# Optimization experiments

Hardware: AMD Instinct MI355X
Metric: run time of the kernel (lower is better)

Reference implementation:

```python
import jax, jax.numpy as jnp
import numpy as np

K_NEIGHBORS = 16
BN_EPS = 1e-5


def _bn(h, g, b):
    # train-mode BatchNorm1d over (batch, points) per channel, biased variance
    mu = h.mean(axis=(0, 1))
    var = h.var(axis=(0, 1))
    return g * (h - mu) * jax.lax.rsqrt(var + BN_EPS) + b


def _gather(arr, idx):
    # arr: [B,N,D], idx: [B,N,K] -> [B,N,K,D]
    return jax.vmap(lambda a, i: a[i])(arr, idx)


def setup_inputs() -> dict:
    key = jax.random.key(0)
    ks = jax.random.split(key, 16)
    B, N, Cin, C, H, M = 4, 4096, 64, 64, 32, 4
    rn = lambda k, s: jax.random.normal(k, s, dtype=jnp.float32) * 0.05
    return {
        "x": jax.random.normal(ks[0], (B, N, Cin), dtype=jnp.float32),
        "p": jax.random.normal(ks[1], (B, N, 3), dtype=jnp.float32),
        "fc1_w": rn(ks[2], (Cin, C)), "fc1_b": jnp.zeros((C,), jnp.float32),
        "bn1_g": jnp.ones((C,), jnp.float32), "bn1_b": jnp.zeros((C,), jnp.float32),
        "qkv_w": rn(ks[3], (C, 3 * C)),
        "pos_w1": rn(ks[4], (3, H)), "pos_b1": jnp.zeros((H,), jnp.float32),
        "pos_w2": rn(ks[5], (H, C)), "pos_b2": jnp.zeros((C,), jnp.float32),
        "attn_w1": rn(ks[6], (C, M * C)), "attn_b1": jnp.zeros((M * C,), jnp.float32),
        "attn_w2": rn(ks[7], (M * C, C)), "attn_b2": jnp.zeros((C,), jnp.float32),
        "bn2_g": jnp.ones((C,), jnp.float32), "bn2_b": jnp.zeros((C,), jnp.float32),
        "fc2_w": rn(ks[8], (C, C)), "fc2_b": jnp.zeros((C,), jnp.float32),
        "bn3_g": jnp.ones((C,), jnp.float32), "bn3_b": jnp.zeros((C,), jnp.float32),
    }


def reference(x, p, fc1_w, fc1_b, bn1_g, bn1_b, qkv_w,
              pos_w1, pos_b1, pos_w2, pos_b2,
              attn_w1, attn_b1, attn_w2, attn_b2,
              bn2_g, bn2_b, fc2_w, fc2_b, bn3_g, bn3_b):
    C = fc1_w.shape[1]
    # fc1 -> BN -> ReLU
    h = jax.nn.relu(_bn(x @ fc1_w + fc1_b, bn1_g, bn1_b))
    residual = h

    # PointTransformerLayer (vector attention over kNN; mask is all-ones)
    qkv = h @ qkv_w  # [B,N,3C]
    q, k, v = qkv[..., :C], qkv[..., C:2 * C], qkv[..., 2 * C:]
    # squared pairwise distances (matches norm-based topk ranking)
    sq = jnp.sum(p * p, axis=-1)  # [B,N]
    d2 = sq[:, :, None] + sq[:, None, :] - 2.0 * jnp.einsum('bnd,bmd->bnm', p, p)
    _, idx = jax.lax.top_k(-d2, K_NEIGHBORS)  # k smallest distances, [B,N,K]

    kj = _gather(k, idx)          # [B,N,K,C]
    vj = _gather(v, idx)          # [B,N,K,C]
    pj = _gather(p, idx)          # [B,N,K,3]

    rel_pos = p[:, :, None, :] - pj                      # [B,N,K,3]
    pe = jax.nn.relu(rel_pos @ pos_w1 + pos_b1) @ pos_w2 + pos_b2  # [B,N,K,C]

    qk_rel = q[:, :, None, :] - kj                       # [B,N,K,C]
    vv = vj + pe
    sim = jax.nn.relu((qk_rel + pe) @ attn_w1 + attn_b1) @ attn_w2 + attn_b2
    attn = jax.nn.softmax(sim, axis=2)                   # softmax over neighbors
    agg = jnp.sum(attn * vv, axis=2)                     # [B,N,C]

    h2 = jax.nn.relu(_bn(agg, bn2_g, bn2_b))
    y = jax.nn.relu(_bn((h2 + residual) @ fc2_w + fc2_b, bn3_g, bn3_b))
    return (y, p)
```

## Files before the change

### kernel.cpp

```cpp
#include <hip/hip_runtime.h>
#include <math.h>

constexpr int kB = 4, kN = 4096, kK = 16;
constexpr int kRows = kB * kN;
constexpr float kEps = 1e-5f;
constexpr float kFltMax = 3.402823466e38f;
constexpr int kCap = 240;

typedef __attribute__((ext_vector_type(8))) short short8;
typedef __attribute__((ext_vector_type(4))) float f32x4;

__device__ __forceinline__ unsigned short f2bf(float x) {
  return (unsigned short)((__float_as_uint(x) + 0x8000u) >> 16);
}
__device__ __forceinline__ unsigned int pkbf(float lo, float hi) {
  return ((__float_as_uint(lo) + 0x8000u) >> 16) |
         ((__float_as_uint(hi) + 0x8000u) & 0xffff0000u);
}
__device__ __forceinline__ float bflo(unsigned int u) { return __uint_as_float(u << 16); }
__device__ __forceinline__ float bfhi(unsigned int u) { return __uint_as_float(u & 0xffff0000u); }
__device__ __forceinline__ float bfu16(unsigned short us) {
  return __uint_as_float(((unsigned int)us) << 16);
}
__device__ __forceinline__ short8 pack8f(float4 a, float4 b) {
  union { unsigned int u[4]; short8 s; } pk;
  pk.u[0] = pkbf(a.x, a.y);
  pk.u[1] = pkbf(a.z, a.w);
  pk.u[2] = pkbf(b.x, b.y);
  pk.u[3] = pkbf(b.z, b.w);
  return pk.s;
}

__device__ __forceinline__ int lane_prefix(unsigned long long m) {
  return __builtin_amdgcn_mbcnt_hi((unsigned)(m >> 32),
         __builtin_amdgcn_mbcnt_lo((unsigned)m, 0));
}

__device__ __forceinline__ void bitonic64(float& sv, int& si, int lane) {
  #pragma unroll
  for (int k = 2; k <= 64; k <<= 1) {
    #pragma unroll
    for (int j = k >> 1; j > 0; j >>= 1) {
      float ov = __shfl_xor(sv, j);
      int   oi = __shfl_xor(si, j);
      bool up = ((lane & k) == 0);
      bool lower = ((lane & j) == 0);
      bool osm = (ov < sv) || (ov == sv && oi < si);
      bool take = (lower == up) ? osm : !osm;
      if (take) { sv = ov; si = oi; }
    }
  }
}

__device__ __forceinline__ float d2q(const float4& Q, const float4& C) {
  float dt = fmaf(Q.z, C.z, fmaf(Q.y, C.y, Q.x * C.x));
  return fmaf(-2.0f, dt, Q.w + C.w);
}

__global__ __launch_bounds__(256) void fc1_conv_kernel(
    const float* __restrict__ x, const float* __restrict__ w,
    const float* __restrict__ bias,
    const float* __restrict__ aw1, const float* __restrict__ aw2,
    const float* __restrict__ pw2, const float* __restrict__ qw,
    const float* __restrict__ f2w,
    const float* __restrict__ pin, float* __restrict__ p4o,
    unsigned short* __restrict__ wpak,
    float* __restrict__ out) {
  __shared__ unsigned short wf[8 * 512];
  const int t = threadIdx.x;
  const int blk = blockIdx.x;
  {
    int id = blk * 256 + t;
    if (id < 16384) {
      int j = id & 7, lane = (id >> 3) & 63, rest = id >> 9;
      int mt = rest >> 1, hh = rest & 1;
      wpak[id] = f2bf(aw1[(32 * hh + 8 * (lane >> 4) + j) * 256 + mt * 16 + (lane & 15)]);
      float3 pp = *reinterpret_cast<const float3*>(pin + 3 * id);
      float4 o;
      o.x = pp.x; o.y = pp.y; o.z = pp.z;
      o.w = pp.x * pp.x + pp.y * pp.y + pp.z * pp.z;
      *reinterpret_cast<float4*>(p4o + 4 * id) = o;
    } else if (id < 32768) {
      int i = id - 16384;
      int j = i & 7, lane = (i >> 3) & 63, rest = i >> 9;
      int ct = rest >> 3, f = rest & 7;
      wpak[id] = f2bf(aw2[(32 * f + 8 * (lane >> 4) + j) * 64 + ct * 16 + (lane & 15)]);
    } else if (id < 34816) {
      int i = id - 32768;
      int c = i >> 5, hh = i & 31;
      wpak[id] = f2bf(pw2[hh * 64 + c]);
    } else if (id < 47104) {
      int i = id - 34816;
      int j = i & 7, lane = (i >> 3) & 63, rest = i >> 9;
      int ct = rest >> 1, hh = rest & 1;
      wpak[id] = f2bf(qw[(32 * hh + 8 * (lane >> 4) + j) * 192 + ct * 16 + (lane & 15)]);
    } else if (id < 51200) {
      int i = id - 47104;
      int j = i & 7, lane = (i >> 3) & 63, rest = i >> 9;
      int ct = rest >> 1, hh = rest & 1;
      wpak[id] = f2bf(f2w[(32 * hh + 8 * (lane >> 4) + j) * 64 + ct * 16 + (lane & 15)]);
    }
  }
  for (int i = t; i < 4096; i += 256) {
    int j = i & 7, lane = (i >> 3) & 63, rest = i >> 9;
    int ct = rest >> 1, hh = rest & 1;
    wf[i] = f2bf(w[(32 * hh + 8 * (lane >> 4) + j) * 64 + ct * 16 + (lane & 15)]);
  }
  __syncthreads();
  const int lane = t & 63, wv = t >> 6;
  const int l = lane & 15, q = lane >> 4;
  const int r0 = blk * 64;
  const int row = r0 + wv * 16 + l;
  const f32x4 zero = {0.f, 0.f, 0.f, 0.f};
  float4 xa0 = *reinterpret_cast<const float4*>(&x[row * 64 + q * 8]);
  float4 xa1 = *reinterpret_cast<const float4*>(&x[row * 64 + q * 8 + 4]);
  float4 xb0 = *reinterpret_cast<const float4*>(&x[row * 64 + 32 + q * 8]);
  float4 xb1 = *reinterpret_cast<const float4*>(&x[row * 64 + 32 + q * 8 + 4]);
  short8 a0 = pack8f(xa0, xa1), a1 = pack8f(xb0, xb1);
  #pragma unroll
  for (int ct = 0; ct < 4; ++ct) {
    short8 b0 = *reinterpret_cast<const short8*>(&wf[(ct * 2 + 0) * 512 + lane * 8]);
    short8 b1 = *reinterpret_cast<const short8*>(&wf[(ct * 2 + 1) * 512 + lane * 8]);
    f32x4 acc = __builtin_amdgcn_mfma_f32_16x16x32_bf16(a0, b0, zero, 0, 0, 0);
    acc = __builtin_amdgcn_mfma_f32_16x16x32_bf16(a1, b1, acc, 0, 0, 0);
    const float bc = bias[ct * 16 + l];
    #pragma unroll
    for (int i = 0; i < 4; ++i)
      out[(r0 + wv * 16 + q * 4 + i) * 64 + ct * 16 + l] = acc[i] + bc;
  }
}

__global__ void stats_part_kernel(const float* __restrict__ src, float* __restrict__ part) {
  __shared__ float sb[256], sb2[256];
  const int t = threadIdx.x, blk = blockIdx.x;
  const int c = t & 63, rg = t >> 6;
  float s = 0.f, s2 = 0.f;
  for (int r = rg; r < 64; r += 4) {
    float v = src[(blk * 64 + r) * 64 + c];
    s += v; s2 += v * v;
  }
  sb[t] = s; sb2[t] = s2; __syncthreads();
  if (t < 64) {
    float ts  = sb[t] + sb[64 + t] + sb[128 + t] + sb[192 + t];
    float ts2 = sb2[t] + sb2[64 + t] + sb2[128 + t] + sb2[192 + t];
    part[blk * 128 + t] = ts;
    part[blk * 128 + 64 + t] = ts2;
  }
}

__global__ void stats_fin_kernel(const float* __restrict__ part,
                                 const float* __restrict__ g, const float* __restrict__ b,
                                 float* __restrict__ A, float* __restrict__ Bv) {
  const int c = threadIdx.x;
  double s = 0.0, s2 = 0.0;
  for (int i = 0; i < 256; ++i) { s += part[i * 128 + c]; s2 += part[i * 128 + 64 + c]; }
  double mean = s / (double)kRows;
  double var = s2 / (double)kRows - mean * mean;
  float rs = (float)(1.0 / sqrt(var + (double)kEps));
  float Af = g[c] * rs;
  A[c] = Af;
  Bv[c] = b[c] - (float)mean * Af;
}

__global__ __launch_bounds__(256) void qkv_bn_kernel(
    const float* __restrict__ hpre, const float* __restrict__ A1,
    const float* __restrict__ B1, const unsigned short* __restrict__ wqf,
    float* __restrict__ hout, unsigned short* __restrict__ out) {
  const int t = threadIdx.x, lane = t & 63, wv = t >> 6;
  const int l = lane & 15, q = lane >> 4;
  const int r0 = blockIdx.x * 64;
  const int row = r0 + wv * 16 + l;
  const f32x4 zero = {0.f, 0.f, 0.f, 0.f};
  short8 af[2];
  #pragma unroll
  for (int hh = 0; hh < 2; ++hh) {
    const int c0 = 32 * hh + q * 8;
    float4 v0 = *reinterpret_cast<const float4*>(&hpre[row * 64 + c0]);
    float4 v1 = *reinterpret_cast<const float4*>(&hpre[row * 64 + c0 + 4]);
    float4 Aa = *reinterpret_cast<const float4*>(&A1[c0]);
    float4 Ab = *reinterpret_cast<const float4*>(&A1[c0 + 4]);
    float4 Ba = *reinterpret_cast<const float4*>(&B1[c0]);
    float4 Bb = *reinterpret_cast<const float4*>(&B1[c0 + 4]);
    v0.x = fmaxf(Aa.x * v0.x + Ba.x, 0.f); v0.y = fmaxf(Aa.y * v0.y + Ba.y, 0.f);
    v0.z = fmaxf(Aa.z * v0.z + Ba.z, 0.f); v0.w = fmaxf(Aa.w * v0.w + Ba.w, 0.f);
    v1.x = fmaxf(Ab.x * v1.x + Bb.x, 0.f); v1.y = fmaxf(Ab.y * v1.y + Bb.y, 0.f);
    v1.z = fmaxf(Ab.z * v1.z + Bb.z, 0.f); v1.w = fmaxf(Ab.w * v1.w + Bb.w, 0.f);
    *reinterpret_cast<float4*>(&hout[row * 64 + c0]) = v0;
    *reinterpret_cast<float4*>(&hout[row * 64 + c0 + 4]) = v1;
    af[hh] = pack8f(v0, v1);
  }
  #pragma unroll
  for (int ct = 0; ct < 12; ++ct) {
    short8 b0 = *reinterpret_cast<const short8*>(&wqf[((ct * 2 + 0) * 64 + lane) * 8]);
    short8 b1 = *reinterpret_cast<const short8*>(&wqf[((ct * 2 + 1) * 64 + lane) * 8]);
    f32x4 acc = __builtin_amdgcn_mfma_f32_16x16x32_bf16(af[0], b0, zero, 0, 0, 0);
    acc = __builtin_amdgcn_mfma_f32_16x16x32_bf16(af[1], b1, acc, 0, 0, 0);
    #pragma unroll
    for (int i = 0; i < 4; ++i)
      out[(r0 + wv * 16 + q * 4 + i) * 192 + ct * 16 + l] = f2bf(acc[i]);
  }
}

__global__ __launch_bounds__(256, 4) void knn_attn_kernel(
    const float* __restrict__ p4, const unsigned short* __restrict__ qkv,
    const float* __restrict__ pos_w1, const float* __restrict__ pos_b1,
    const float* __restrict__ pos_b2,
    const float* __restrict__ attn_b1, const float* __restrict__ attn_b2,
    const unsigned short* __restrict__ w1f,
    const unsigned short* __restrict__ w2f,
    const unsigned short* __restrict__ pw2t,
    float* __restrict__ agg) {
  __shared__ unsigned short Ulds[64 * 72];
  __shared__ unsigned short VVb[64 * 72];
  __shared__ float sthr[4];
  __shared__ int   scnt[4];

  const int t = threadIdx.x;
  const int lane = t & 63, w = t >> 6;
  const int l = lane & 15, q = lane >> 4;
  const int work = ((blockIdx.x & 7) << 9) | (blockIdx.x >> 3);
  const int b = work >> 10;
  const int pt_row = work * 4 + w;
  const int qrow0 = work * 4;
  const int base = b * kN;
  const f32x4 zero = {0.f, 0.f, 0.f, 0.f};

  if (t < 4) scnt[t] = 0;

  const float4 q0f = *reinterpret_cast<const float4*>(p4 + 4 * (qrow0 + 0));
  const float4 q1f = *reinterpret_cast<const float4*>(p4 + 4 * (qrow0 + 1));
  const float4 q2f = *reinterpret_cast<const float4*>(p4 + 4 * (qrow0 + 2));
  const float4 q3f = *reinterpret_cast<const float4*>(p4 + 4 * (qrow0 + 3));
  const float4 qp4 = *reinterpret_cast<const float4*>(p4 + 4 * pt_row);
  const float qx = qp4.x, qy = qp4.y, qz = qp4.z, sqq = qp4.w;

  unsigned pk0[8], pk1[8], pk2[8], pk3[8];
  float lmin = kFltMax;
  const int cbase = base + w * 1024;
  #pragma unroll
  for (int g = 0; g < 2; ++g) {
    float4 cc[8];
    #pragma unroll
    for (int jj = 0; jj < 8; ++jj)
      cc[jj] = *reinterpret_cast<const float4*>(p4 + 4 * (cbase + (g * 8 + jj) * 64 + lane));
    #pragma unroll
    for (int jj = 0; jj < 8; ++jj) {
      float dot = fmaf(qz, cc[jj].z, fmaf(qy, cc[jj].y, qx * cc[jj].x));
      lmin = fminf(lmin, fmaf(-2.0f, dot, sqq + cc[jj].w));
    }
    #pragma unroll
    for (int pi = 0; pi < 4; ++pi) {
      const float4 ca = cc[2 * pi], cb = cc[2 * pi + 1];
      pk0[g * 4 + pi] = (__float_as_uint(d2q(q0f, ca)) >> 16) |
                        (__float_as_uint(d2q(q0f, cb)) & 0xffff0000u);
      pk1[g * 4 + pi] = (__float_as_uint(d2q(q1f, ca)) >> 16) |
                        (__float_as_uint(d2q(q1f, cb)) & 0xffff0000u);
      pk2[g * 4 + pi] = (__float_as_uint(d2q(q2f, ca)) >> 16) |
                        (__float_as_uint(d2q(q2f, cb)) & 0xffff0000u);
      pk3[g * 4 + pi] = (__float_as_uint(d2q(q3f, ca)) >> 16) |
                        (__float_as_uint(d2q(q3f, cb)) & 0xffff0000u);
    }
  }
  {
    int dummy = lane;
    float lm = lmin;
    bitonic64(lm, dummy, lane);
    float s16 = __shfl(lm, 15);
    if (lane == 0) sthr[w] = s16 + 1e-3f;
  }
  __syncthreads();

  {
    auto append_q = [&](const unsigned (&PK)[8], int j) {
      int* listj = reinterpret_cast<int*>(VVb) + j * 576;
      const float thrj = sthr[j];
      #pragma unroll
      for (int g = 0; g < 2; ++g) {
        unsigned long long m[8];
        int pc[8];
        #pragma unroll
        for (int c = 0; c < 8; ++c) {
          unsigned pku = PK[g * 4 + (c >> 1)];
          float dv = (c & 1) ? __uint_as_float(pku & 0xffff0000u)
                             : __uint_as_float(pku << 16);
          m[c] = __ballot(dv <= thrj);
          pc[c] = __popcll(m[c]);
        }
        int tot = pc[0] + pc[1] + pc[2] + pc[3] + pc[4] + pc[5] + pc[6] + pc[7];
        int old = 0;
        if (lane == 0) old = atomicAdd(&scnt[j], tot);
        old = __shfl(old, 0);
        int pre = 0;
        #pragma unroll
        for (int c = 0; c < 8; ++c) {
          if ((m[c] >> lane) & 1ull) {
            int pos = old + pre + lane_prefix(m[c]);
            if (pos < kCap) listj[pos] = w * 1024 + (g * 8 + c) * 64 + lane;
          }
          pre += pc[c];
        }
      }
    };
    append_q(pk0, 0);
    append_q(pk1, 1);
    append_q(pk2, 2);
    append_q(pk3, 3);
  }
  __syncthreads();

  const int n = scnt[w];
  const int* bufi = reinterpret_cast<const int*>(VVb) + w * 576;
  float sv = kFltMax;
  int   si = 0x7fffffff;
  if (n <= kCap) {
    for (int g0 = 0; g0 < n; g0 += 48) {
      float mv; int mi;
      if (lane < 16) { mv = sv; mi = si; }
      else {
        int pos = g0 + (lane - 16);
        if (pos < n) {
          int jj = bufi[pos];
          float4 c = *reinterpret_cast<const float4*>(p4 + 4 * (base + jj));
          mv = d2q(qp4, c);
          mi = jj;
        } else { mv = kFltMax; mi = 0x7fffffff; }
      }
      bitonic64(mv, mi, lane);
      sv = mv; si = mi;
    }
  } else {
    for (int g0 = 0; g0 < kN; g0 += 48) {
      float mv; int mi;
      if (lane < 16) { mv = sv; mi = si; }
      else {
        int j = g0 + (lane - 16);
        if (j < kN) {
          float4 c = *reinterpret_cast<const float4*>(p4 + 4 * (base + j));
          mv = d2q(qp4, c);
          mi = j;
        } else { mv = kFltMax; mi = 0x7fffffff; }
      }
      bitonic64(mv, mi, lane);
      sv = mv; si = mi;
    }
  }

  int idxv = 0;
  if (lane < 16) {
    int o = si;
    if ((unsigned)o >= (unsigned)kN) o = 0;
    idxv = o;
  }

  asm volatile("" ::: "memory");

  {
    const int r = lane >> 2, seg = lane & 3;
    const unsigned short* jrow = qkv + (base + __shfl(idxv, r)) * 192;
    const int c0 = seg * 16;
    uint4 k0 = *reinterpret_cast<const uint4*>(jrow + 64 + c0);
    uint4 k1 = *reinterpret_cast<const uint4*>(jrow + 64 + c0 + 8);
    uint4 v0 = *reinterpret_cast<const uint4*>(jrow + 128 + c0);
    uint4 v1 = *reinterpret_cast<const uint4*>(jrow + 128 + c0 + 8);
    uint4 q0 = *reinterpret_cast<const uint4*>(qkv + pt_row * 192 + c0);
    uint4 q1 = *reinterpret_cast<const uint4*>(qkv + pt_row * 192 + c0 + 8);
    auto diff2 = [](unsigned int qu, unsigned int ku) -> unsigned int {
      float lo = bflo(qu) - bflo(ku);
      float hi = bfhi(qu) - bfhi(ku);
      return pkbf(lo, hi);
    };
    uint4 u0, u1;
    u0.x = diff2(q0.x, k0.x); u0.y = diff2(q0.y, k0.y);
    u0.z = diff2(q0.z, k0.z); u0.w = diff2(q0.w, k0.w);
    u1.x = diff2(q1.x, k1.x); u1.y = diff2(q1.y, k1.y);
    u1.z = diff2(q1.z, k1.z); u1.w = diff2(q1.w, k1.w);
    *reinterpret_cast<uint4*>(&Ulds[(w * 16 + r) * 72 + c0]) = u0;
    *reinterpret_cast<uint4*>(&Ulds[(w * 16 + r) * 72 + c0 + 8]) = u1;
    *reinterpret_cast<uint4*>(&VVb[(w * 16 + r) * 72 + c0]) = v0;
    *reinterpret_cast<uint4*>(&VVb[(w * 16 + r) * 72 + c0 + 8]) = v1;
  }
  short8 pbf;
  {
    const int nj = __shfl(idxv, l);
    const float4 pj4 = *reinterpret_cast<const float4*>(p4 + 4 * (base + nj));
    float rx = qx - pj4.x, ry = qy - pj4.y, rz = qz - pj4.z;
    float hv[8];
    #pragma unroll
    for (int j = 0; j < 8; ++j) {
      int hh = q * 8 + j;
      hv[j] = fmaxf(pos_b1[hh] + rx * pos_w1[hh] + ry * pos_w1[32 + hh] +
                    rz * pos_w1[64 + hh], 0.0f);
    }
    union { unsigned int u[4]; short8 s; } pk;
    #pragma unroll
    for (int ii = 0; ii < 4; ++ii) pk.u[ii] = pkbf(hv[2 * ii], hv[2 * ii + 1]);
    pbf = pk.s;
  }

  {
    const int urow = (w * 16 + l) * 72;
    #pragma unroll
    for (int mt = 0; mt < 4; ++mt) {
      short8 paf = *reinterpret_cast<const short8*>(&pw2t[(mt * 16 + l) * 32 + q * 8]);
      f32x4 pe = __builtin_amdgcn_mfma_f32_16x16x32_bf16(paf, pbf, zero, 0, 0, 0);
      const int c0 = mt * 16 + q * 4;
      float4 b2v = *reinterpret_cast<const float4*>(&pos_b2[c0]);
      float pe0 = pe[0] + b2v.x, pe1 = pe[1] + b2v.y;
      float pe2 = pe[2] + b2v.z, pe3 = pe[3] + b2v.w;
      uint2 u2 = *reinterpret_cast<uint2*>(&Ulds[urow + c0]);
      uint2 o;
      o.x = pkbf(bflo(u2.x) + pe0, bfhi(u2.x) + pe1);
      o.y = pkbf(bflo(u2.y) + pe2, bfhi(u2.y) + pe3);
      *reinterpret_cast<uint2*>(&Ulds[urow + c0]) = o;
      uint2 v2 = *reinterpret_cast<uint2*>(&VVb[urow + c0]);
      uint2 ov;
      ov.x = pkbf(bflo(v2.x) + pe0, bfhi(v2.x) + pe1);
      ov.y = pkbf(bflo(v2.y) + pe2, bfhi(v2.y) + pe3);
      *reinterpret_cast<uint2*>(&VVb[urow + c0]) = ov;
    }
  }

  {
    f32x4 acc2[4];
    #pragma unroll
    for (int ct = 0; ct < 4; ++ct) acc2[ct] = zero;
    const int urow = (w * 16 + l) * 72;
    short8 ub0 = *reinterpret_cast<const short8*>(&Ulds[urow + q * 8]);
    short8 ub1 = *reinterpret_cast<const short8*>(&Ulds[urow + 32 + q * 8]);
    const int sbase = l + 32 * (q & 1);
    const bool hi_mt = (q >= 2);
    #pragma unroll
    for (int f = 0; f < 8; ++f) {
      unsigned plo2[2], phi2[2];
      #pragma unroll
      for (int s = 0; s < 2; ++s) {
        const int mt = 2 * f + s;
        short8 a0 = *reinterpret_cast<const short8*>(&w1f[(mt * 2 + 0) * 512 + lane * 8]);
        short8 a1 = *reinterpret_cast<const short8*>(&w1f[(mt * 2 + 1) * 512 + lane * 8]);
        f32x4 acc = __builtin_amdgcn_mfma_f32_16x16x32_bf16(a0, ub0, zero, 0, 0, 0);
        acc = __builtin_amdgcn_mfma_f32_16x16x32_bf16(a1, ub1, acc, 0, 0, 0);
        float4 bb = *reinterpret_cast<const float4*>(&attn_b1[mt * 16 + q * 4]);
        plo2[s] = pkbf(fmaxf(acc[0] + bb.x, 0.f), fmaxf(acc[1] + bb.y, 0.f));
        phi2[s] = pkbf(fmaxf(acc[2] + bb.z, 0.f), fmaxf(acc[3] + bb.w, 0.f));
      }
      union { unsigned int u[4]; short8 s; } pk;
      #pragma unroll
      for (int d = 0; d < 4; ++d) {
        const int src = sbase + ((d >> 1) << 4);
        const unsigned int w0 = (d & 1) ? phi2[0] : plo2[0];
        const unsigned int w1v = (d & 1) ? phi2[1] : plo2[1];
        unsigned int va = (unsigned int)__shfl((int)w0, src);
        unsigned int vb = (unsigned int)__shfl((int)w1v, src);
        pk.u[d] = hi_mt ? vb : va;
      }
      short8 afr = pk.s;
      #pragma unroll
      for (int ct = 0; ct < 4; ++ct) {
        short8 bfr = *reinterpret_cast<const short8*>(&w2f[((ct * 8 + f) * 64 + lane) * 8]);
        acc2[ct] = __builtin_amdgcn_mfma_f32_16x16x32_bf16(afr, bfr, acc2[ct], 0, 0, 0);
      }
    }
    #pragma unroll
    for (int ct = 0; ct < 4; ++ct) {
      const int ch = ct * 16 + l;
      const float bv = attn_b2[ch];
      float s0v = acc2[ct][0] + bv, s1v = acc2[ct][1] + bv;
      float s2v = acc2[ct][2] + bv, s3v = acc2[ct][3] + bv;
      float mx = fmaxf(fmaxf(s0v, s1v), fmaxf(s2v, s3v));
      mx = fmaxf(mx, __shfl_xor(mx, 16, 64));
      mx = fmaxf(mx, __shfl_xor(mx, 32, 64));
      float e0 = __expf(s0v - mx), e1 = __expf(s1v - mx);
      float e2 = __expf(s2v - mx), e3 = __expf(s3v - mx);
      float se = e0 + e1 + e2 + e3;
      se += __shfl_xor(se, 16, 64);
      se += __shfl_xor(se, 32, 64);
      const int vbase = (w * 16 + q * 4) * 72 + ch;
      float a = e0 * bfu16(VVb[vbase])       + e1 * bfu16(VVb[vbase + 72]) +
                e2 * bfu16(VVb[vbase + 144]) + e3 * bfu16(VVb[vbase + 216]);
      a += __shfl_xor(a, 16, 64);
      a += __shfl_xor(a, 32, 64);
      if (q == 0) agg[pt_row * 64 + ch] = a / se;
    }
  }
}

__global__ __launch_bounds__(256) void fc2_mfma_kernel(
    const float* __restrict__ aggp, const float* __restrict__ hres,
    const float* __restrict__ A2, const float* __restrict__ B2,
    const unsigned short* __restrict__ fc2f, const float* __restrict__ bias,
    float* __restrict__ z) {
  const int t = threadIdx.x, lane = t & 63, wv = t >> 6;
  const int l = lane & 15, q = lane >> 4;
  const int r0 = blockIdx.x * 64;
  const int row = r0 + wv * 16 + l;
  const f32x4 zero = {0.f, 0.f, 0.f, 0.f};
  short8 af[2];
  #pragma unroll
  for (int hh = 0; hh < 2; ++hh) {
    const int c0 = 32 * hh + q * 8;
    float4 v0 = *reinterpret_cast<const float4*>(&aggp[row * 64 + c0]);
    float4 v1 = *reinterpret_cast<const float4*>(&aggp[row * 64 + c0 + 4]);
    float4 r0v = *reinterpret_cast<const float4*>(&hres[row * 64 + c0]);
    float4 r1v = *reinterpret_cast<const float4*>(&hres[row * 64 + c0 + 4]);
    float4 Aa = *reinterpret_cast<const float4*>(&A2[c0]);
    float4 Ab = *reinterpret_cast<const float4*>(&A2[c0 + 4]);
    float4 Ba = *reinterpret_cast<const float4*>(&B2[c0]);
    float4 Bb = *reinterpret_cast<const float4*>(&B2[c0 + 4]);
    v0.x = fmaxf(Aa.x * v0.x + Ba.x, 0.f) + r0v.x;
    v0.y = fmaxf(Aa.y * v0.y + Ba.y, 0.f) + r0v.y;
    v0.z = fmaxf(Aa.z * v0.z + Ba.z, 0.f) + r0v.z;
    v0.w = fmaxf(Aa.w * v0.w + Ba.w, 0.f) + r0v.w;
    v1.x = fmaxf(Ab.x * v1.x + Bb.x, 0.f) + r1v.x;
    v1.y = fmaxf(Ab.y * v1.y + Bb.y, 0.f) + r1v.y;
    v1.z = fmaxf(Ab.z * v1.z + Bb.z, 0.f) + r1v.z;
    v1.w = fmaxf(Ab.w * v1.w + Bb.w, 0.f) + r1v.w;
    af[hh] = pack8f(v0, v1);
  }
  #pragma unroll
  for (int ct = 0; ct < 4; ++ct) {
    short8 b0 = *reinterpret_cast<const short8*>(&fc2f[((ct * 2 + 0) * 64 + lane) * 8]);
    short8 b1 = *reinterpret_cast<const short8*>(&fc2f[((ct * 2 + 1) * 64 + lane) * 8]);
    f32x4 acc = __builtin_amdgcn_mfma_f32_16x16x32_bf16(af[0], b0, zero, 0, 0, 0);
    acc = __builtin_amdgcn_mfma_f32_16x16x32_bf16(af[1], b1, acc, 0, 0, 0);
    const float bc = bias[ct * 16 + l];
    #pragma unroll
    for (int i = 0; i < 4; ++i)
      z[(r0 + wv * 16 + q * 4 + i) * 64 + ct * 16 + l] = acc[i] + bc;
  }
}

__global__ void final_kernel(const float* __restrict__ z, const float* __restrict__ A3,
                             const float* __restrict__ B3, const float* __restrict__ p,
                             float* __restrict__ y) {
  const int blk = blockIdx.x, t = threadIdx.x;
  if (blk < 4096) {
    int i = blk * 256 + t;
    int c = i & 63;
    y[i] = fmaxf(A3[c] * z[i] + B3[c], 0.0f);
  } else {
    int i = (blk - 4096) * 256 + t;
    y[1048576 + i] = p[i];
  }
}

extern "C" void kernel_launch(void* const* d_in, const int* in_sizes, int n_in,
                              void* d_out, int out_size, void* d_ws, size_t ws_size,
                              hipStream_t stream) {
  const float* x       = (const float*)d_in[0];
  const float* p       = (const float*)d_in[1];
  const float* fc1_w   = (const float*)d_in[2];
  const float* fc1_b   = (const float*)d_in[3];
  const float* bn1_g   = (const float*)d_in[4];
  const float* bn1_b   = (const float*)d_in[5];
  const float* qkv_w   = (const float*)d_in[6];
  const float* pos_w1  = (const float*)d_in[7];
  const float* pos_b1  = (const float*)d_in[8];
  const float* pos_w2  = (const float*)d_in[9];
  const float* pos_b2  = (const float*)d_in[10];
  const float* attn_w1 = (const float*)d_in[11];
  const float* attn_b1 = (const float*)d_in[12];
  const float* attn_w2 = (const float*)d_in[13];
  const float* attn_b2 = (const float*)d_in[14];
  const float* bn2_g   = (const float*)d_in[15];
  const float* bn2_b   = (const float*)d_in[16];
  const float* fc2_w   = (const float*)d_in[17];
  const float* fc2_b   = (const float*)d_in[18];
  const float* bn3_g   = (const float*)d_in[19];
  const float* bn3_b   = (const float*)d_in[20];

  float* ws   = (float*)d_ws;
  float* h    = ws;
  unsigned short* qkvb = (unsigned short*)(ws + 1048576);
  float* hpre = ws + 4194304;
  float* aggv = ws + 5242880;
  float* z    = ws + 6291456;
  float* st   = ws + 7340032;
  float* p4   = ws + 7356800;
  unsigned short* wpak = (unsigned short*)(ws + 7618944);
  unsigned short* w1f  = wpak;
  unsigned short* w2f  = wpak + 16384;
  unsigned short* pw2t = wpak + 32768;
  unsigned short* wqf  = wpak + 34816;
  unsigned short* fc2f = wpak + 47104;

  float* A1 = st,       *B1 = st + 64;
  float* A2 = st + 128, *B2 = st + 192;
  float* A3 = st + 256, *B3 = st + 320;
  float* y = (float*)d_out;

  fc1_conv_kernel<<<256, 256, 0, stream>>>(x, fc1_w, fc1_b, attn_w1, attn_w2,
                                           pos_w2, qkv_w, fc2_w, p, p4, wpak, hpre);
  stats_part_kernel<<<256, 256, 0, stream>>>(hpre, aggv);
  stats_fin_kernel<<<1, 64, 0, stream>>>(aggv, bn1_g, bn1_b, A1, B1);
  qkv_bn_kernel<<<256, 256, 0, stream>>>(hpre, A1, B1, wqf, h, qkvb);
  knn_attn_kernel<<<4096, 256, 0, stream>>>(p4, qkvb, pos_w1, pos_b1, pos_b2,
                                            attn_b1, attn_b2, w1f, w2f, pw2t, aggv);
  stats_part_kernel<<<256, 256, 0, stream>>>(aggv, z);
  stats_fin_kernel<<<1, 64, 0, stream>>>(z, bn2_g, bn2_b, A2, B2);
  fc2_mfma_kernel<<<256, 256, 0, stream>>>(aggv, h, A2, B2, fc2f, fc2_b, z);
  stats_part_kernel<<<256, 256, 0, stream>>>(z, aggv);
  stats_fin_kernel<<<1, 64, 0, stream>>>(aggv, bn3_g, bn3_b, A3, B3);
  final_kernel<<<4288, 256, 0, stream>>>(z, A3, B3, p, y);
}
```

Baseline: 268.0 us.

## Fuse BN partial stats into fc1/fc2 GEMMs and split blocks per column tile

```diff
diff --git a/kernel.cpp b/kernel.cpp
--- a/kernel.cpp
+++ b/kernel.cpp
@@ -65,8 +65,9 @@
     const float* __restrict__ f2w,
     const float* __restrict__ pin, float* __restrict__ p4o,
     unsigned short* __restrict__ wpak,
-    float* __restrict__ out) {
+    float* __restrict__ out, float* __restrict__ part) {
   __shared__ unsigned short wf[8 * 512];
+  __shared__ float S[64][5], S2[64][5];
   const int t = threadIdx.x;
   const int blk = blockIdx.x;
   {
@@ -109,24 +110,32 @@
   __syncthreads();
   const int lane = t & 63, wv = t >> 6;
   const int l = lane & 15, q = lane >> 4;
-  const int r0 = blk * 64;
-  const int row = r0 + wv * 16 + l;
+  const int r0 = blk * 16;
+  const int row = r0 + l;
   const f32x4 zero = {0.f, 0.f, 0.f, 0.f};
   float4 xa0 = *reinterpret_cast<const float4*>(&x[row * 64 + q * 8]);
   float4 xa1 = *reinterpret_cast<const float4*>(&x[row * 64 + q * 8 + 4]);
   float4 xb0 = *reinterpret_cast<const float4*>(&x[row * 64 + 32 + q * 8]);
   float4 xb1 = *reinterpret_cast<const float4*>(&x[row * 64 + 32 + q * 8 + 4]);
   short8 a0 = pack8f(xa0, xa1), a1 = pack8f(xb0, xb1);
+  const int ct = wv;
+  short8 b0 = *reinterpret_cast<const short8*>(&wf[(ct * 2 + 0) * 512 + lane * 8]);
+  short8 b1 = *reinterpret_cast<const short8*>(&wf[(ct * 2 + 1) * 512 + lane * 8]);
+  f32x4 acc = __builtin_amdgcn_mfma_f32_16x16x32_bf16(a0, b0, zero, 0, 0, 0);
+  acc = __builtin_amdgcn_mfma_f32_16x16x32_bf16(a1, b1, acc, 0, 0, 0);
+  const float bc = bias[ct * 16 + l];
+  float s = 0.f, s2 = 0.f;
   #pragma unroll
-  for (int ct = 0; ct < 4; ++ct) {
-    short8 b0 = *reinterpret_cast<const short8*>(&wf[(ct * 2 + 0) * 512 + lane * 8]);
-    short8 b1 = *reinterpret_cast<const short8*>(&wf[(ct * 2 + 1) * 512 + lane * 8]);
-    f32x4 acc = __builtin_amdgcn_mfma_f32_16x16x32_bf16(a0, b0, zero, 0, 0, 0);
-    acc = __builtin_amdgcn_mfma_f32_16x16x32_bf16(a1, b1, acc, 0, 0, 0);
-    const float bc = bias[ct * 16 + l];
-    #pragma unroll
-    for (int i = 0; i < 4; ++i)
-      out[(r0 + wv * 16 + q * 4 + i) * 64 + ct * 16 + l] = acc[i] + bc;
+  for (int i = 0; i < 4; ++i) {
+    float v = acc[i] + bc;
+    out[(r0 + q * 4 + i) * 64 + ct * 16 + l] = v;
+    s += v; s2 += v * v;
+  }
+  S[ct * 16 + l][q] = s; S2[ct * 16 + l][q] = s2;
+  __syncthreads();
+  if (t < 64) {
+    part[blk * 128 + t]      = S[t][0] + S[t][1] + S[t][2] + S[t][3];
+    part[blk * 128 + 64 + t] = S2[t][0] + S2[t][1] + S2[t][2] + S2[t][3];
   }
 }
 
@@ -150,16 +159,29 @@
 
 __global__ void stats_fin_kernel(const float* __restrict__ part,
                                  const float* __restrict__ g, const float* __restrict__ b,
-                                 float* __restrict__ A, float* __restrict__ Bv) {
-  const int c = threadIdx.x;
+                                 float* __restrict__ A, float* __restrict__ Bv, int cnt) {
+  __shared__ double ds[256], ds2[256];
+  const int t = threadIdx.x;
+  const int c = t & 63, grp = t >> 6;
+  const int per = cnt >> 2;
   double s = 0.0, s2 = 0.0;
-  for (int i = 0; i < 256; ++i) { s += part[i * 128 + c]; s2 += part[i * 128 + 64 + c]; }
-  double mean = s / (double)kRows;
-  double var = s2 / (double)kRows - mean * mean;
-  float rs = (float)(1.0 / sqrt(var + (double)kEps));
-  float Af = g[c] * rs;
-  A[c] = Af;
-  Bv[c] = b[c] - (float)mean * Af;
+  for (int k = 0; k < per; ++k) {
+    int i = grp * per + k;
+    s  += part[i * 128 + c];
+    s2 += part[i * 128 + 64 + c];
+  }
+  ds[grp * 64 + c] = s; ds2[grp * 64 + c] = s2;
+  __syncthreads();
+  if (t < 64) {
+    double ts  = ds[t] + ds[64 + t] + ds[128 + t] + ds[192 + t];
+    double ts2 = ds2[t] + ds2[64 + t] + ds2[128 + t] + ds2[192 + t];
+    double mean = ts / (double)kRows;
+    double var = ts2 / (double)kRows - mean * mean;
+    float rs = (float)(1.0 / sqrt(var + (double)kEps));
+    float Af = g[t] * rs;
+    A[t] = Af;
+    Bv[t] = b[t] - (float)mean * Af;
+  }
 }
 
 __global__ __launch_bounds__(256) void qkv_bn_kernel(
@@ -168,8 +190,8 @@
     float* __restrict__ hout, unsigned short* __restrict__ out) {
   const int t = threadIdx.x, lane = t & 63, wv = t >> 6;
   const int l = lane & 15, q = lane >> 4;
-  const int r0 = blockIdx.x * 64;
-  const int row = r0 + wv * 16 + l;
+  const int r0 = blockIdx.x * 16;
+  const int row = r0 + l;
   const f32x4 zero = {0.f, 0.f, 0.f, 0.f};
   short8 af[2];
   #pragma unroll
@@ -185,19 +207,22 @@
     v0.z = fmaxf(Aa.z * v0.z + Ba.z, 0.f); v0.w = fmaxf(Aa.w * v0.w + Ba.w, 0.f);
     v1.x = fmaxf(Ab.x * v1.x + Bb.x, 0.f); v1.y = fmaxf(Ab.y * v1.y + Bb.y, 0.f);
     v1.z = fmaxf(Ab.z * v1.z + Bb.z, 0.f); v1.w = fmaxf(Ab.w * v1.w + Bb.w, 0.f);
-    *reinterpret_cast<float4*>(&hout[row * 64 + c0]) = v0;
-    *reinterpret_cast<float4*>(&hout[row * 64 + c0 + 4]) = v1;
+    if (wv == 0) {
+      *reinterpret_cast<float4*>(&hout[row * 64 + c0]) = v0;
+      *reinterpret_cast<float4*>(&hout[row * 64 + c0 + 4]) = v1;
+    }
     af[hh] = pack8f(v0, v1);
   }
   #pragma unroll
-  for (int ct = 0; ct < 12; ++ct) {
+  for (int s = 0; s < 3; ++s) {
+    const int ct = wv * 3 + s;
     short8 b0 = *reinterpret_cast<const short8*>(&wqf[((ct * 2 + 0) * 64 + lane) * 8]);
     short8 b1 = *reinterpret_cast<const short8*>(&wqf[((ct * 2 + 1) * 64 + lane) * 8]);
     f32x4 acc = __builtin_amdgcn_mfma_f32_16x16x32_bf16(af[0], b0, zero, 0, 0, 0);
     acc = __builtin_amdgcn_mfma_f32_16x16x32_bf16(af[1], b1, acc, 0, 0, 0);
     #pragma unroll
     for (int i = 0; i < 4; ++i)
-      out[(r0 + wv * 16 + q * 4 + i) * 192 + ct * 16 + l] = f2bf(acc[i]);
+      out[(r0 + q * 4 + i) * 192 + ct * 16 + l] = f2bf(acc[i]);
   }
 }
 
@@ -488,11 +513,12 @@
     const float* __restrict__ aggp, const float* __restrict__ hres,
     const float* __restrict__ A2, const float* __restrict__ B2,
     const unsigned short* __restrict__ fc2f, const float* __restrict__ bias,
-    float* __restrict__ z) {
+    float* __restrict__ z, float* __restrict__ part) {
+  __shared__ float S[64][5], S2[64][5];
   const int t = threadIdx.x, lane = t & 63, wv = t >> 6;
   const int l = lane & 15, q = lane >> 4;
-  const int r0 = blockIdx.x * 64;
-  const int row = r0 + wv * 16 + l;
+  const int r0 = blockIdx.x * 16;
+  const int row = r0 + l;
   const f32x4 zero = {0.f, 0.f, 0.f, 0.f};
   short8 af[2];
   #pragma unroll
@@ -516,16 +542,24 @@
     v1.w = fmaxf(Ab.w * v1.w + Bb.w, 0.f) + r1v.w;
     af[hh] = pack8f(v0, v1);
   }
+  const int ct = wv;
+  short8 b0 = *reinterpret_cast<const short8*>(&fc2f[((ct * 2 + 0) * 64 + lane) * 8]);
+  short8 b1 = *reinterpret_cast<const short8*>(&fc2f[((ct * 2 + 1) * 64 + lane) * 8]);
+  f32x4 acc = __builtin_amdgcn_mfma_f32_16x16x32_bf16(af[0], b0, zero, 0, 0, 0);
+  acc = __builtin_amdgcn_mfma_f32_16x16x32_bf16(af[1], b1, acc, 0, 0, 0);
+  const float bc = bias[ct * 16 + l];
+  float s = 0.f, s2 = 0.f;
   #pragma unroll
-  for (int ct = 0; ct < 4; ++ct) {
-    short8 b0 = *reinterpret_cast<const short8*>(&fc2f[((ct * 2 + 0) * 64 + lane) * 8]);
-    short8 b1 = *reinterpret_cast<const short8*>(&fc2f[((ct * 2 + 1) * 64 + lane) * 8]);
-    f32x4 acc = __builtin_amdgcn_mfma_f32_16x16x32_bf16(af[0], b0, zero, 0, 0, 0);
-    acc = __builtin_amdgcn_mfma_f32_16x16x32_bf16(af[1], b1, acc, 0, 0, 0);
-    const float bc = bias[ct * 16 + l];
-    #pragma unroll
-    for (int i = 0; i < 4; ++i)
-      z[(r0 + wv * 16 + q * 4 + i) * 64 + ct * 16 + l] = acc[i] + bc;
+  for (int i = 0; i < 4; ++i) {
+    float v = acc[i] + bc;
+    z[(r0 + q * 4 + i) * 64 + ct * 16 + l] = v;
+    s += v; s2 += v * v;
+  }
+  S[ct * 16 + l][q] = s; S2[ct * 16 + l][q] = s2;
+  __syncthreads();
+  if (t < 64) {
+    part[blockIdx.x * 128 + t]      = S[t][0] + S[t][1] + S[t][2] + S[t][3];
+    part[blockIdx.x * 128 + 64 + t] = S2[t][0] + S2[t][1] + S2[t][2] + S2[t][3];
   }
 }
 
@@ -588,17 +622,16 @@
   float* A3 = st + 256, *B3 = st + 320;
   float* y = (float*)d_out;
 
-  fc1_conv_kernel<<<256, 256, 0, stream>>>(x, fc1_w, fc1_b, attn_w1, attn_w2,
-                                           pos_w2, qkv_w, fc2_w, p, p4, wpak, hpre);
-  stats_part_kernel<<<256, 256, 0, stream>>>(hpre, aggv);
-  stats_fin_kernel<<<1, 64, 0, stream>>>(aggv, bn1_g, bn1_b, A1, B1);
-  qkv_bn_kernel<<<256, 256, 0, stream>>>(hpre, A1, B1, wqf, h, qkvb);
+  fc1_conv_kernel<<<1024, 256, 0, stream>>>(x, fc1_w, fc1_b, attn_w1, attn_w2,
+                                            pos_w2, qkv_w, fc2_w, p, p4, wpak,
+                                            hpre, aggv);
+  stats_fin_kernel<<<1, 256, 0, stream>>>(aggv, bn1_g, bn1_b, A1, B1, 1024);
+  qkv_bn_kernel<<<1024, 256, 0, stream>>>(hpre, A1, B1, wqf, h, qkvb);
   knn_attn_kernel<<<4096, 256, 0, stream>>>(p4, qkvb, pos_w1, pos_b1, pos_b2,
                                             attn_b1, attn_b2, w1f, w2f, pw2t, aggv);
   stats_part_kernel<<<256, 256, 0, stream>>>(aggv, z);
-  stats_fin_kernel<<<1, 64, 0, stream>>>(z, bn2_g, bn2_b, A2, B2);
-  fc2_mfma_kernel<<<256, 256, 0, stream>>>(aggv, h, A2, B2, fc2f, fc2_b, z);
-  stats_part_kernel<<<256, 256, 0, stream>>>(z, aggv);
-  stats_fin_kernel<<<1, 64, 0, stream>>>(aggv, bn3_g, bn3_b, A3, B3);
+  stats_fin_kernel<<<1, 256, 0, stream>>>(z, bn2_g, bn2_b, A2, B2, 256);
+  fc2_mfma_kernel<<<1024, 256, 0, stream>>>(aggv, h, A2, B2, fc2f, fc2_b, z, hpre);
+  stats_fin_kernel<<<1, 256, 0, stream>>>(hpre, bn3_g, bn3_b, A3, B3, 1024);
   final_kernel<<<4288, 256, 0, stream>>>(z, A3, B3, p, y);
 }
```

Measured after the change: 378.2 us. 1.41x slower.
